# Optimization experiments

Hardware: AMD Instinct MI355X
Metric: run time of the kernel (lower is better)

The kernel has to match this reference:

```python
import jax, jax.numpy as jnp
import numpy as np


def setup_inputs() -> dict:
    key = jax.random.key(0)
    kq, kk, kv, km = jax.random.split(key, 4)
    B, H, S, D = 2, 16, 2048, 64
    Q = jax.random.normal(kq, (B, H, S, D), dtype=jnp.float32)
    K = jax.random.normal(kk, (B, H, S, D), dtype=jnp.float32)
    V = jax.random.normal(kv, (B, H, S, D), dtype=jnp.float32)
    attn_mask = jax.random.randint(km, (B, 1, S, S), 0, 2).astype(jnp.bool_)
    return {"Q": Q, "K": K, "V": V, "attn_mask": attn_mask}


def reference(Q, K, V, attn_mask):
    d_k = Q.shape[-1]
    # scores = Q @ K^T / sqrt(d_k)  -> [B, H, S, S]
    scores = jnp.einsum('bhqd,bhkd->bhqk', Q, K) / jnp.sqrt(jnp.float32(d_k))
    # faithful to torch masked_fill_(attn_mask, 1e-9): masked positions set to 1e-9
    scores = jnp.where(attn_mask, jnp.float32(1e-9), scores)
    attn = jax.nn.softmax(scores, axis=-1)
    context = jnp.einsum('bhqk,bhkd->bhqd', attn, V)
    return (context, attn)
```

## Files before the change

### kernel.cpp

```cpp
#include <hip/hip_runtime.h>

#define BB 2
#define HH 16
#define SS 2048
#define DD 64

typedef __attribute__((ext_vector_type(8))) _Float16 half8;
typedef __attribute__((ext_vector_type(4))) float f32x4;

__device__ __forceinline__ half8 cvt8(f32x4 a, f32x4 b) {
  half8 r;
  r[0] = (_Float16)a[0]; r[1] = (_Float16)a[1];
  r[2] = (_Float16)a[2]; r[3] = (_Float16)a[3];
  r[4] = (_Float16)b[0]; r[5] = (_Float16)b[1];
  r[6] = (_Float16)b[2]; r[7] = (_Float16)b[3];
  return r;
}

__global__ __launch_bounds__(512, 4)
void sdpa_kernel(const float* __restrict__ Q, const float* __restrict__ K,
                 const float* __restrict__ V, const void* __restrict__ M,
                 float* __restrict__ out_ctx, float* __restrict__ out_attn) {
  __shared__ _Float16 E[16 * 2048];
  __shared__ float zacc[8][16];
  __shared__ f32x4 pscr[4][64];

  const int bh   = blockIdx.y;
  const int b    = bh >> 4;
  const int q0   = blockIdx.x << 4;
  const int tid  = threadIdx.x;
  const int wave = tid >> 6;
  const int lane = tid & 63;
  const int col  = lane & 15;
  const int quad = lane >> 4;

  const unsigned int* mw = (const unsigned int*)M;
  unsigned int probe = mw[lane];
  unsigned long long bi = __ballot(probe <= 1u);
  unsigned long long bf = __ballot(probe == 0u || probe == 0x3f800000u);
  const int mmode = (bi == ~0ull) ? 0 : ((bf == ~0ull) ? 1 : 2);
  const int*           m32 = (const int*)M           + (size_t)b * SS * SS;
  const float*         mfp = (const float*)M         + (size_t)b * SS * SS;
  const unsigned char* m8  = (const unsigned char*)M + (size_t)b * SS * SS;

  const float* Qb = Q + (size_t)bh * SS * DD;
  const float* Kb = K + (size_t)bh * SS * DD;
  const float* Vb = V + (size_t)bh * SS * DD;

  half8 aQ0, aQ1;
  {
    const float* qp = Qb + (size_t)(q0 + col) * DD + quad * 8;
    f32x4 x0 = *(const f32x4*)(qp);
    f32x4 x1 = *(const f32x4*)(qp + 4);
    f32x4 x2 = *(const f32x4*)(qp + 32);
    f32x4 x3 = *(const f32x4*)(qp + 36);
    aQ0 = cvt8(x0, x1);
    aQ1 = cvt8(x2, x3);
  }

  float zpart[4] = {0.f, 0.f, 0.f, 0.f};
#pragma unroll 2
  for (int n0 = wave * 16; n0 < SS; n0 += 128) {
    const float* kp = Kb + (size_t)(n0 + col) * DD + quad * 8;
    f32x4 x0 = *(const f32x4*)(kp);
    f32x4 x1 = *(const f32x4*)(kp + 4);
    f32x4 x2 = *(const f32x4*)(kp + 32);
    f32x4 x3 = *(const f32x4*)(kp + 36);
    half8 bK0 = cvt8(x0, x1);
    half8 bK1 = cvt8(x2, x3);
    f32x4 c = {0.f, 0.f, 0.f, 0.f};
    c = __builtin_amdgcn_mfma_f32_16x16x32_f16(aQ0, bK0, c, 0, 0, 0);
    c = __builtin_amdgcn_mfma_f32_16x16x32_f16(aQ1, bK1, c, 0, 0, 0);
    const int key = n0 + col;
#pragma unroll
    for (int r = 0; r < 4; ++r) {
      const int row = quad * 4 + r;
      const size_t midx = (size_t)(q0 + row) * SS + key;
      int mv;
      if (mmode == 0)      mv = m32[midx];
      else if (mmode == 1) mv = (mfp[midx] != 0.f);
      else                 mv = m8[midx];
      const float sc = mv ? 1e-9f : c[r] * 0.125f;
      const float e  = __expf(sc);
      zpart[r] += e;
      const int gp = (key >> 3) ^ (row & 7);
      E[row * 2048 + gp * 8 + (key & 7)] = (_Float16)e;
    }
  }
#pragma unroll
  for (int r = 0; r < 4; ++r) {
    float z = zpart[r];
    z += __shfl_xor(z, 1, 64);
    z += __shfl_xor(z, 2, 64);
    z += __shfl_xor(z, 4, 64);
    z += __shfl_xor(z, 8, 64);
    if (col == 0) zacc[wave][quad * 4 + r] = z;
  }
  __syncthreads();

  const int d0 = (wave & 3) << 4;
  const int h  = wave >> 2;
  const int kbase = h << 10;
  f32x4 u = {0.f, 0.f, 0.f, 0.f};
#pragma unroll 2
  for (int kk = 0; kk < 1024; kk += 32) {
    const int kk0 = kbase + kk;
    const int gp = ((kk0 + quad * 8) >> 3) ^ (col & 7);
    half8 aP = *(const half8*)&E[col * 2048 + gp * 8];
    const float* vp = Vb + (size_t)(kk0 + quad * 8) * DD + d0 + col;
    half8 bV;
#pragma unroll
    for (int jj = 0; jj < 8; ++jj) bV[jj] = (_Float16)vp[(size_t)jj * DD];
    u = __builtin_amdgcn_mfma_f32_16x16x32_f16(aP, bV, u, 0, 0, 0);
  }
  if (h) pscr[wave & 3][lane] = u;
  __syncthreads();

  if (h == 0) {
    f32x4 u2 = pscr[wave][lane];
#pragma unroll
    for (int r = 0; r < 4; ++r) {
      const int row = quad * 4 + r;
      float z = 0.f;
#pragma unroll
      for (int w = 0; w < 8; ++w) z += zacc[w][row];
      out_ctx[((size_t)bh * SS + (q0 + row)) * DD + d0 + col] = (u[r] + u2[r]) / z;
    }
  }

#pragma unroll
  for (int rr = 0; rr < 2; ++rr) {
    const int row = (wave << 1) + rr;
    float z = 0.f;
#pragma unroll
    for (int w = 0; w < 8; ++w) z += zacc[w][row];
    const float rz = 1.0f / z;
    float* arow = out_attn + ((size_t)bh * SS + (q0 + row)) * SS;
#pragma unroll
    for (int i = 0; i < 4; ++i) {
      const int gpr = i * 64 + lane;
      half8 v = *(const half8*)&E[row * 2048 + gpr * 8];
      const int gcol = i * 64 + (lane ^ (row & 7));
      f32x4 w0, w1;
#pragma unroll
      for (int j = 0; j < 4; ++j) {
        w0[j] = (float)v[j] * rz;
        w1[j] = (float)v[j + 4] * rz;
      }
      __builtin_nontemporal_store(w0, (f32x4*)(arow + gcol * 8));
      __builtin_nontemporal_store(w1, (f32x4*)(arow + gcol * 8 + 4));
    }
  }
}

extern "C" void kernel_launch(void* const* d_in, const int* in_sizes, int n_in,
                              void* d_out, int out_size, void* d_ws, size_t ws_size,
                              hipStream_t stream) {
  const float* Q = (const float*)d_in[0];
  const float* K = (const float*)d_in[1];
  const float* V = (const float*)d_in[2];
  const void*  M = d_in[3];
  float* ctx  = (float*)d_out;
  float* attn = ctx + (size_t)BB * HH * SS * DD;
  dim3 grid(SS / 16, BB * HH);
  sdpa_kernel<<<grid, 512, 0, stream>>>(Q, K, V, M, ctx, attn);
}
```

Measured before the change: 1.047 ms.

## Pack mask into LDS bitmask and interleave attn stores with PV loop

The mask tile for the block's 16 rows is now loaded with coalesced vector loads before the score loop, compressed to bits with LDS atomics, and read back from LDS there. This replaces the scattered per-element global mask reads. The attention-matrix write-out is moved into the P·V loop, one chunk every fourth iteration, so stores overlap with MFMA and V loads. Plain stores replace the nontemporal ones, and the unroll factors are raised. The cost is an extra barrier pass, LDS atomics, and a larger LDS footprint, which may reduce occupancy.

```diff
diff --git a/kernel.cpp b/kernel.cpp
--- a/kernel.cpp
+++ b/kernel.cpp
@@ -7,6 +7,7 @@
 
 typedef __attribute__((ext_vector_type(8))) _Float16 half8;
 typedef __attribute__((ext_vector_type(4))) float f32x4;
+typedef __attribute__((ext_vector_type(4))) unsigned int u32x4;
 
 __device__ __forceinline__ half8 cvt8(f32x4 a, f32x4 b) {
   half8 r;
@@ -22,6 +23,7 @@
                  const float* __restrict__ V, const void* __restrict__ M,
                  float* __restrict__ out_ctx, float* __restrict__ out_attn) {
   __shared__ _Float16 E[16 * 2048];
+  __shared__ unsigned int mbits[16][64];
   __shared__ float zacc[8][16];
   __shared__ f32x4 pscr[4][64];
 
@@ -39,9 +41,6 @@
   unsigned long long bi = __ballot(probe <= 1u);
   unsigned long long bf = __ballot(probe == 0u || probe == 0x3f800000u);
   const int mmode = (bi == ~0ull) ? 0 : ((bf == ~0ull) ? 1 : 2);
-  const int*           m32 = (const int*)M           + (size_t)b * SS * SS;
-  const float*         mfp = (const float*)M         + (size_t)b * SS * SS;
-  const unsigned char* m8  = (const unsigned char*)M + (size_t)b * SS * SS;
 
   const float* Qb = Q + (size_t)bh * SS * DD;
   const float* Kb = K + (size_t)bh * SS * DD;
@@ -58,8 +57,49 @@
     aQ1 = cvt8(x2, x3);
   }
 
+  {
+    unsigned int* mflat = &mbits[0][0];
+    mflat[tid] = 0u;
+    mflat[tid + 512] = 0u;
+    __syncthreads();
+    if (mmode == 2) {
+      const unsigned char* mb = (const unsigned char*)M + (size_t)b * SS * SS + (size_t)q0 * SS;
+#pragma unroll
+      for (int j = 0; j < 4; ++j) {
+        const int lin = (tid + j * 512) * 16;
+        u32x4 v = *(const u32x4*)(mb + lin);
+        unsigned int bits = 0;
+#pragma unroll
+        for (int w = 0; w < 4; ++w) {
+          unsigned int x = v[w];
+          bits |= ((x & 0x000000ffu) ? 1u : 0u) << (w * 4 + 0);
+          bits |= ((x & 0x0000ff00u) ? 1u : 0u) << (w * 4 + 1);
+          bits |= ((x & 0x00ff0000u) ? 1u : 0u) << (w * 4 + 2);
+          bits |= ((x & 0xff000000u) ? 1u : 0u) << (w * 4 + 3);
+        }
+        const int row = lin >> 11, key0 = lin & 2047;
+        atomicOr(&mbits[row][key0 >> 5], bits << (key0 & 31));
+      }
+    } else {
+      const unsigned int* mv4 = (const unsigned int*)M + (size_t)b * SS * SS + (size_t)q0 * SS;
+#pragma unroll
+      for (int j = 0; j < 16; ++j) {
+        const int lin = (tid + j * 512) * 4;
+        u32x4 v = *(const u32x4*)(mv4 + lin);
+        unsigned int bits = 0;
+        bits |= v[0] ? 1u : 0u;
+        bits |= v[1] ? 2u : 0u;
+        bits |= v[2] ? 4u : 0u;
+        bits |= v[3] ? 8u : 0u;
+        const int row = lin >> 11, key0 = lin & 2047;
+        atomicOr(&mbits[row][key0 >> 5], bits << (key0 & 31));
+      }
+    }
+    __syncthreads();
+  }
+
   float zpart[4] = {0.f, 0.f, 0.f, 0.f};
-#pragma unroll 2
+#pragma unroll 4
   for (int n0 = wave * 16; n0 < SS; n0 += 128) {
     const float* kp = Kb + (size_t)(n0 + col) * DD + quad * 8;
     f32x4 x0 = *(const f32x4*)(kp);
@@ -71,15 +111,13 @@
     f32x4 c = {0.f, 0.f, 0.f, 0.f};
     c = __builtin_amdgcn_mfma_f32_16x16x32_f16(aQ0, bK0, c, 0, 0, 0);
     c = __builtin_amdgcn_mfma_f32_16x16x32_f16(aQ1, bK1, c, 0, 0, 0);
-    const int key = n0 + col;
+    const int key    = n0 + col;
+    const int mword  = n0 >> 5;
+    const int mshift = (n0 & 16) + col;
 #pragma unroll
     for (int r = 0; r < 4; ++r) {
       const int row = quad * 4 + r;
-      const size_t midx = (size_t)(q0 + row) * SS + key;
-      int mv;
-      if (mmode == 0)      mv = m32[midx];
-      else if (mmode == 1) mv = (mfp[midx] != 0.f);
-      else                 mv = m8[midx];
+      const int mv = (mbits[row][mword] >> mshift) & 1;
       const float sc = mv ? 1e-9f : c[r] * 0.125f;
       const float e  = __expf(sc);
       zpart[r] += e;
@@ -101,10 +139,19 @@
   const int d0 = (wave & 3) << 4;
   const int h  = wave >> 2;
   const int kbase = h << 10;
+  float rzr[2];
+#pragma unroll
+  for (int rr = 0; rr < 2; ++rr) {
+    const int row = (wave << 1) + rr;
+    float z = 0.f;
+#pragma unroll
+    for (int w = 0; w < 8; ++w) z += zacc[w][row];
+    rzr[rr] = 1.0f / z;
+  }
   f32x4 u = {0.f, 0.f, 0.f, 0.f};
-#pragma unroll 2
-  for (int kk = 0; kk < 1024; kk += 32) {
-    const int kk0 = kbase + kk;
+#pragma unroll 4
+  for (int t = 0; t < 32; ++t) {
+    const int kk0 = kbase + t * 32;
     const int gp = ((kk0 + quad * 8) >> 3) ^ (col & 7);
     half8 aP = *(const half8*)&E[col * 2048 + gp * 8];
     const float* vp = Vb + (size_t)(kk0 + quad * 8) * DD + d0 + col;
@@ -112,6 +159,24 @@
 #pragma unroll
     for (int jj = 0; jj < 8; ++jj) bV[jj] = (_Float16)vp[(size_t)jj * DD];
     u = __builtin_amdgcn_mfma_f32_16x16x32_f16(aP, bV, u, 0, 0, 0);
+    if ((t & 3) == 3) {
+      const int g   = t >> 2;
+      const int rr  = g >> 2;
+      const int i   = g & 3;
+      const int row = (wave << 1) + rr;
+      const int gpr = i * 64 + lane;
+      half8 v = *(const half8*)&E[row * 2048 + gpr * 8];
+      const int gcol = i * 64 + (lane ^ (row & 7));
+      float* arow = out_attn + ((size_t)bh * SS + (q0 + row)) * SS;
+      f32x4 w0, w1;
+#pragma unroll
+      for (int j = 0; j < 4; ++j) {
+        w0[j] = (float)v[j] * rzr[rr];
+        w1[j] = (float)v[j + 4] * rzr[rr];
+      }
+      *(f32x4*)(arow + gcol * 8)     = w0;
+      *(f32x4*)(arow + gcol * 8 + 4) = w1;
+    }
   }
   if (h) pscr[wave & 3][lane] = u;
   __syncthreads();
@@ -125,30 +190,6 @@
 #pragma unroll
       for (int w = 0; w < 8; ++w) z += zacc[w][row];
       out_ctx[((size_t)bh * SS + (q0 + row)) * DD + d0 + col] = (u[r] + u2[r]) / z;
-    }
-  }
-
-#pragma unroll
-  for (int rr = 0; rr < 2; ++rr) {
-    const int row = (wave << 1) + rr;
-    float z = 0.f;
-#pragma unroll
-    for (int w = 0; w < 8; ++w) z += zacc[w][row];
-    const float rz = 1.0f / z;
-    float* arow = out_attn + ((size_t)bh * SS + (q0 + row)) * SS;
-#pragma unroll
-    for (int i = 0; i < 4; ++i) {
-      const int gpr = i * 64 + lane;
-      half8 v = *(const half8*)&E[row * 2048 + gpr * 8];
-      const int gcol = i * 64 + (lane ^ (row & 7));
-      f32x4 w0, w1;
-#pragma unroll
-      for (int j = 0; j < 4; ++j) {
-        w0[j] = (float)v[j] * rz;
-        w1[j] = (float)v[j + 4] * rz;
-      }
-      __builtin_nontemporal_store(w0, (f32x4*)(arow + gcol * 8));
-      __builtin_nontemporal_store(w1, (f32x4*)(arow + gcol * 8 + 4));
     }
   }
 }
```

Result: faster. 965.5 us (-7.8%).
